# Performance work log

Hardware: AMD Instinct MI355X
Metric: run time of the kernel (lower is better)

## Reference

```python
import jax, jax.numpy as jnp
import numpy as np

PIECES = 64  # self.plane


def _proj(f, w1, b1, w2, b2):
    # Projection: fc2(relu(fc1(f))), final_relu=False
    h = jax.nn.relu(f @ w1 + b1)
    return h @ w2 + b2


def _cf(img, param, pieces):
    # img: [B,3,H,W], param: [B,3,P]
    # total[b,c,h,w] = sum_i clamp(img - i/P, 0, 1/P) * param[b,c,i], then * P / sum_i param
    grid = jnp.arange(pieces, dtype=img.dtype) / pieces            # [P]
    clipped = jnp.clip(img[..., None] - grid, 0.0, 1.0 / pieces)   # [B,3,H,W,P]
    total = jnp.einsum('bchwp,bcp->bchw', clipped, param)
    norm = pieces / (jnp.sum(param, axis=-1) + 1e-30)              # [B,3]
    return total * norm[:, :, None, None]


def setup_inputs() -> dict:
    key = jax.random.key(0)
    ks = jax.random.split(key, 11)
    B, H, W = 8, 256, 256
    s = 0.05
    return {
        'x': jax.random.uniform(ks[0], (B, 3, H, W), jnp.float32),
        'f_feature': jax.random.normal(ks[1], (B, 512), jnp.float32),
        'b_feature': jax.random.normal(ks[2], (B, 512), jnp.float32),
        # stacked weights for [fc_f_1, fc_b_1, fc_f_s, fc_b_s]
        'proj_w1': jax.random.normal(ks[3], (4, 512, 192), jnp.float32) * s,
        'proj_b1': jax.random.normal(ks[4], (4, 192), jnp.float32) * s,
        'proj_w2': jax.random.normal(ks[5], (4, 192, 192), jnp.float32) * s,
        'proj_b2': jax.random.normal(ks[6], (4, 192), jnp.float32) * s,
        'fc_w1': jax.random.normal(ks[7], (576, 192), jnp.float32) * s,
        'fc_b1': jax.random.normal(ks[8], (192,), jnp.float32) * s,
        'fc_w2': jax.random.normal(ks[9], (192, 192), jnp.float32) * s,
        'fc_b2': jax.random.normal(ks[10], (192,), jnp.float32) * s,
    }


def reference(x, f_feature, b_feature, proj_w1, proj_b1, proj_w2, proj_b2,
              fc_w1, fc_b1, fc_w2, fc_b2):
    B = x.shape[0]
    # rgb_to_grayscale with 3 output channels (ITU-R 601 weights)
    gw = jnp.array([0.299, 0.587, 0.114], dtype=x.dtype)
    gray = jnp.broadcast_to(jnp.einsum('bchw,c->bhw', x, gw)[:, None], x.shape)

    # four stacked Projections: inputs [f, b, f, b]
    feats = jnp.stack([f_feature, b_feature, f_feature, b_feature])       # [4,B,512]
    h = jax.nn.relu(jnp.einsum('kbi,kio->kbo', feats, proj_w1) + proj_b1[:, None, :])
    outs = jnp.einsum('kbo,koq->kbq', h, proj_w2) + proj_b2[:, None, :]   # [4,B,192]
    param_f, param_b = outs[0], outs[1]
    param_s = outs[2] + outs[3]

    cat = jnp.concatenate([param_f, param_b, param_s], axis=1)            # [B,576]
    param = _proj(cat, fc_w1, fc_b1, fc_w2, fc_b2)                        # [B,192]

    p_all = param.reshape(B, 3, PIECES)
    p_f = param_f.reshape(B, 3, PIECES)
    p_b = param_b.reshape(B, 3, PIECES)

    return (_cf(x, p_all, PIECES), _cf(gray, p_f, PIECES), _cf(gray, p_b, PIECES))
```

## Files before the change

kernel.cpp:

```cpp
#include <hip/hip_runtime.h>

#define HWSZ 65536
#define PLANE (3 * HWSZ)
#define OUTSTRIDE (8 * PLANE)
#define MAGIC 0x13572468

__global__ __launch_bounds__(384) void k_mlp(
    const float* __restrict__ f, const float* __restrict__ bf,
    const float* __restrict__ pw1, const float* __restrict__ pb1,
    const float* __restrict__ pw2, const float* __restrict__ pb2,
    const float* __restrict__ fw1, const float* __restrict__ fb1,
    const float* __restrict__ fw2, const float* __restrict__ fb2,
    float* __restrict__ ws) {
  __shared__ float smem[2304];
  int t = threadIdx.x, blk = blockIdx.x;

  float* outs    = ws;
  float* partial = ws + 8192;
  int* fbase = (int*)(ws + 16384);

  int k = blk >> 3, b = blk & 7;
  {
    int q = t % 48, s = t / 48;
    float* sf  = smem;
    float* red = smem + 512;
    float* sh  = smem + 2048;

    const float* feat = ((k & 1) ? bf : f) + b * 512;
    for (int i = t; i < 512; i += 384) sf[i] = feat[i];
    __syncthreads();

    {
      const float4* w = (const float4*)(pw1 + (size_t)k * (512 * 192));
      float4 acc = {0.f, 0.f, 0.f, 0.f};
      int i0 = s * 64;
      for (int r = 0; r < 4; ++r) {
        float4 wv[16];
#pragma unroll
        for (int j = 0; j < 16; ++j)
          wv[j] = w[(size_t)(i0 + r * 16 + j) * 48 + q];
#pragma unroll
        for (int j = 0; j < 16; ++j) {
          float v = sf[i0 + r * 16 + j];
          acc.x = fmaf(v, wv[j].x, acc.x); acc.y = fmaf(v, wv[j].y, acc.y);
          acc.z = fmaf(v, wv[j].z, acc.z); acc.w = fmaf(v, wv[j].w, acc.w);
        }
      }
      ((float4*)(red + s * 192))[q] = acc;
    }
    __syncthreads();
    if (t < 192) {
      float a = pb1[k * 192 + t];
#pragma unroll
      for (int s2 = 0; s2 < 8; ++s2) a += red[s2 * 192 + t];
      sh[t] = fmaxf(a, 0.f);
    }
    __syncthreads();
    {
      const float4* w = (const float4*)(pw2 + (size_t)k * (192 * 192));
      float4 acc = {0.f, 0.f, 0.f, 0.f};
      int i0 = s * 24;
      for (int r = 0; r < 2; ++r) {
        float4 wv[12];
#pragma unroll
        for (int j = 0; j < 12; ++j)
          wv[j] = w[(size_t)(i0 + r * 12 + j) * 48 + q];
#pragma unroll
        for (int j = 0; j < 12; ++j) {
          float v = sh[i0 + r * 12 + j];
          acc.x = fmaf(v, wv[j].x, acc.x); acc.y = fmaf(v, wv[j].y, acc.y);
          acc.z = fmaf(v, wv[j].z, acc.z); acc.w = fmaf(v, wv[j].w, acc.w);
        }
      }
      ((float4*)(red + s * 192))[q] = acc;
    }
    __syncthreads();
    if (t < 192) {
      float a = pb2[k * 192 + t];
#pragma unroll
      for (int s2 = 0; s2 < 8; ++s2) a += red[s2 * 192 + t];
      outs[(k * 8 + b) * 192 + t] = a;
    }
    __syncthreads();
    if (t == 0) {
      __threadfence();
      atomicExch(&fbase[blk * 16], MAGIC);
    }
  }

  int b2 = blk & 7, c4 = blk >> 3, ob2 = c4 * 48;
  int q = t % 12, s = t / 12;
  int q2 = t % 48, s2 = t / 48;

  float4 wv1[18];
  {
    const float4* w = (const float4*)fw1;
    int i0 = s * 18;
#pragma unroll
    for (int j = 0; j < 18; ++j)
      wv1[j] = w[(size_t)(i0 + j) * 48 + (ob2 >> 2) + q];
  }
  float4 wv2[6];
  {
    const float4* w = (const float4*)fw2;
#pragma unroll
    for (int j = 0; j < 6; ++j)
      wv2[j] = w[(size_t)(ob2 + s2 * 6 + j) * 48 + q2];
  }

  if (t < 4) {
    while (atomicAdd(&fbase[(t * 8 + b2) * 16], 0) != MAGIC)
      __builtin_amdgcn_s_sleep(2);
  }
  __syncthreads();
  if (t == 0) __threadfence();
  __syncthreads();

  {
    float* sc  = smem;
    float* red = smem + 576;
    for (int idx = t; idx < 576; idx += 384) {
      float v;
      if (idx < 192)      v = outs[(0 * 8 + b2) * 192 + idx];
      else if (idx < 384) v = outs[(1 * 8 + b2) * 192 + (idx - 192)];
      else                v = outs[(2 * 8 + b2) * 192 + (idx - 384)] +
                              outs[(3 * 8 + b2) * 192 + (idx - 384)];
      sc[idx] = v;
    }
    __syncthreads();
    {
      float4 acc = {0.f, 0.f, 0.f, 0.f};
      int i0 = s * 18;
#pragma unroll
      for (int j = 0; j < 18; ++j) {
        float v = sc[i0 + j];
        acc.x = fmaf(v, wv1[j].x, acc.x); acc.y = fmaf(v, wv1[j].y, acc.y);
        acc.z = fmaf(v, wv1[j].z, acc.z); acc.w = fmaf(v, wv1[j].w, acc.w);
      }
      ((float4*)(red + s * 48))[q] = acc;
    }
    __syncthreads();
    if (t < 48) {
      float a = fb1[ob2 + t];
#pragma unroll
      for (int s3 = 0; s3 < 32; ++s3) a += red[s3 * 48 + t];
      smem[t] = fmaxf(a, 0.f);
    }
    __syncthreads();
    {
      float4 acc = {0.f, 0.f, 0.f, 0.f};
#pragma unroll
      for (int j = 0; j < 6; ++j) {
        float v = smem[s2 * 6 + j];
        acc.x = fmaf(v, wv2[j].x, acc.x); acc.y = fmaf(v, wv2[j].y, acc.y);
        acc.z = fmaf(v, wv2[j].z, acc.z); acc.w = fmaf(v, wv2[j].w, acc.w);
      }
      ((float4*)(red + s2 * 192))[q2] = acc;
    }
    __syncthreads();
    if (t < 192) {
      float a = (c4 == 0) ? fb2[t] : 0.f;
#pragma unroll
      for (int s3 = 0; s3 < 8; ++s3) a += red[s3 * 192 + t];
      partial[(c4 * 8 + b2) * 192 + t] = a;
    }
  }
}

__global__ __launch_bounds__(256) void k_render(
    const float* __restrict__ x, const float* __restrict__ ws,
    float* __restrict__ out) {
  int b = blockIdx.y, t = threadIdx.x;
  int wave = t >> 6, lane = t & 63;
  const float* outs    = ws;
  const float* partial = ws + 8192;
  __shared__ float2 tab[576];

  int s4a = blockIdx.x * 512 + t, s4b = s4a + 256;
  const float* xb = x + (size_t)b * PLANE;
  float4 vr0 = ((const float4*)(xb))[s4a];
  float4 vr1 = ((const float4*)(xb))[s4b];
  float4 vg0 = ((const float4*)(xb + HWSZ))[s4a];
  float4 vg1 = ((const float4*)(xb + HWSZ))[s4b];
  float4 vb0 = ((const float4*)(xb + 2 * HWSZ))[s4a];
  float4 vb1 = ((const float4*)(xb + 2 * HWSZ))[s4b];

  for (int cur = wave; cur < 9; cur += 4) {
    int oi = cur / 3, c = cur - oi * 3;
    float p;
    if (oi == 0) {
      const float* pp = partial + b * 192 + c * 64;
      p = pp[lane] + pp[1536 + lane] + pp[3072 + lane] + pp[4608 + lane];
    } else {
      p = outs[((oi - 1) * 8 + b) * 192 + c * 64 + lane];
    }
    float v = p;
#pragma unroll
    for (int d = 1; d < 64; d <<= 1) {
      float n = __shfl_up(v, d, 64);
      if (lane >= d) v += n;
    }
    float total = __shfl(v, 63, 64);
    float norm = 64.f / (total + 1e-30f);
    tab[cur * 64 + lane] = make_float2((v - p) * 0.015625f * norm, p * norm);
  }
  __syncthreads();

  auto idx_of = [&](float v, int& kk, float& tt) {
    int k = (int)(v * 64.f);
    k = k < 0 ? 0 : (k > 63 ? 63 : k);
    kk = k;
    tt = v - (float)k * 0.015625f;
  };
  auto evk = [&](int cur, int k, float tt) -> float {
    float2 e = tab[cur * 64 + k];
    return fmaf(tt, e.y, e.x);
  };
  auto ev4 = [&](int cur, float4 v) -> float4 {
    int k; float tt; float4 r;
    idx_of(v.x, k, tt); r.x = evk(cur, k, tt);
    idx_of(v.y, k, tt); r.y = evk(cur, k, tt);
    idx_of(v.z, k, tt); r.z = evk(cur, k, tt);
    idx_of(v.w, k, tt); r.w = evk(cur, k, tt);
    return r;
  };

  float* o0 = out + (size_t)b * PLANE;
  float* o1 = out + OUTSTRIDE + (size_t)b * PLANE;
  float* o2 = out + 2 * OUTSTRIDE + (size_t)b * PLANE;

  auto process = [&](int s4, float4 vr, float4 vg, float4 vb) {
    float4 gr;
    gr.x = fmaf(0.299f, vr.x, fmaf(0.587f, vg.x, 0.114f * vb.x));
    gr.y = fmaf(0.299f, vr.y, fmaf(0.587f, vg.y, 0.114f * vb.y));
    gr.z = fmaf(0.299f, vr.z, fmaf(0.587f, vg.z, 0.114f * vb.z));
    gr.w = fmaf(0.299f, vr.w, fmaf(0.587f, vg.w, 0.114f * vb.w));

    ((float4*)(o0))[s4]            = ev4(0, vr);
    ((float4*)(o0 + HWSZ))[s4]     = ev4(1, vg);
    ((float4*)(o0 + 2 * HWSZ))[s4] = ev4(2, vb);

    int kx, ky, kz, kw; float tx, ty, tz, tw;
    idx_of(gr.x, kx, tx); idx_of(gr.y, ky, ty);
    idx_of(gr.z, kz, tz); idx_of(gr.w, kw, tw);
#pragma unroll
    for (int c = 0; c < 3; ++c) {
      float4 r;
      r.x = evk(3 + c, kx, tx); r.y = evk(3 + c, ky, ty);
      r.z = evk(3 + c, kz, tz); r.w = evk(3 + c, kw, tw);
      ((float4*)(o1 + c * HWSZ))[s4] = r;
    }
#pragma unroll
    for (int c = 0; c < 3; ++c) {
      float4 r;
      r.x = evk(6 + c, kx, tx); r.y = evk(6 + c, ky, ty);
      r.z = evk(6 + c, kz, tz); r.w = evk(6 + c, kw, tw);
      ((float4*)(o2 + c * HWSZ))[s4] = r;
    }
  };

  process(s4a, vr0, vg0, vb0);
  process(s4b, vr1, vg1, vb1);
}

extern "C" void kernel_launch(void* const* d_in, const int* in_sizes, int n_in,
                              void* d_out, int out_size, void* d_ws, size_t ws_size,
                              hipStream_t stream) {
  const float* x   = (const float*)d_in[0];
  const float* f   = (const float*)d_in[1];
  const float* bf  = (const float*)d_in[2];
  const float* pw1 = (const float*)d_in[3];
  const float* pb1 = (const float*)d_in[4];
  const float* pw2 = (const float*)d_in[5];
  const float* pb2 = (const float*)d_in[6];
  const float* fw1 = (const float*)d_in[7];
  const float* fb1 = (const float*)d_in[8];
  const float* fw2 = (const float*)d_in[9];
  const float* fb2 = (const float*)d_in[10];
  float* out = (float*)d_out;
  float* ws  = (float*)d_ws;

  k_mlp<<<32, 384, 0, stream>>>(f, bf, pw1, pb1, pw2, pb2, fw1, fb1, fw2,
                                fb2, ws);
  dim3 grid(32, 8);
  k_render<<<grid, 256, 0, stream>>>(x, ws, out);
}
```

Measured before the change: 97.92 us.

## Split projection MLP hidden dim across two blocks to double MLP parallelism

The projection MLP kernel now launches 64 blocks instead of 32, each computing half of the fc1 hidden units for one (projection, batch) pair and writing a partial fc2 result. The two halves and the fc2 bias are summed by the consumers (the final-fc stage and the render kernel). Only half the blocks continue into the final-fc stage, and each now spin-waits on 8 flags instead of 4. This aims to cut per-block weight streaming latency on the critical path, at the cost of extra partial reads and more inter-block flag synchronization.

```diff
diff --git a/kernel.cpp b/kernel.cpp
--- a/kernel.cpp
+++ b/kernel.cpp
@@ -15,13 +15,13 @@
   __shared__ float smem[2304];
   int t = threadIdx.x, blk = blockIdx.x;
 
-  float* outs    = ws;
-  float* partial = ws + 8192;
-  int* fbase = (int*)(ws + 16384);
-
-  int k = blk >> 3, b = blk & 7;
+  float* pA      = ws;
+  float* partial = ws + 12288;
+  int* fbase = (int*)(ws + 20480);
+
+  int s = blk & 7, b = blk >> 3;
+  int k = s >> 1, half = s & 1, o0 = half * 96;
   {
-    int q = t % 48, s = t / 48;
     float* sf  = smem;
     float* red = smem + 512;
     float* sh  = smem + 2048;
@@ -31,14 +31,16 @@
     __syncthreads();
 
     {
+      int q = t % 24, sr = t / 24;
       const float4* w = (const float4*)(pw1 + (size_t)k * (512 * 192));
+      int icol = half * 24 + q;
       float4 acc = {0.f, 0.f, 0.f, 0.f};
-      int i0 = s * 64;
-      for (int r = 0; r < 4; ++r) {
+      int i0 = sr * 32;
+      for (int r = 0; r < 2; ++r) {
         float4 wv[16];
 #pragma unroll
         for (int j = 0; j < 16; ++j)
-          wv[j] = w[(size_t)(i0 + r * 16 + j) * 48 + q];
+          wv[j] = w[(size_t)(i0 + r * 16 + j) * 48 + icol];
 #pragma unroll
         for (int j = 0; j < 16; ++j) {
           float v = sf[i0 + r * 16 + j];
@@ -46,40 +48,38 @@
           acc.z = fmaf(v, wv[j].z, acc.z); acc.w = fmaf(v, wv[j].w, acc.w);
         }
       }
-      ((float4*)(red + s * 192))[q] = acc;
-    }
-    __syncthreads();
-    if (t < 192) {
-      float a = pb1[k * 192 + t];
-#pragma unroll
-      for (int s2 = 0; s2 < 8; ++s2) a += red[s2 * 192 + t];
+      ((float4*)(red + sr * 96))[q] = acc;
+    }
+    __syncthreads();
+    if (t < 96) {
+      float a = pb1[k * 192 + o0 + t];
+#pragma unroll
+      for (int s2 = 0; s2 < 16; ++s2) a += red[s2 * 96 + t];
       sh[t] = fmaxf(a, 0.f);
     }
     __syncthreads();
     {
+      int q2 = t % 48, s2 = t / 48;
       const float4* w = (const float4*)(pw2 + (size_t)k * (192 * 192));
       float4 acc = {0.f, 0.f, 0.f, 0.f};
-      int i0 = s * 24;
-      for (int r = 0; r < 2; ++r) {
-        float4 wv[12];
-#pragma unroll
-        for (int j = 0; j < 12; ++j)
-          wv[j] = w[(size_t)(i0 + r * 12 + j) * 48 + q];
-#pragma unroll
-        for (int j = 0; j < 12; ++j) {
-          float v = sh[i0 + r * 12 + j];
-          acc.x = fmaf(v, wv[j].x, acc.x); acc.y = fmaf(v, wv[j].y, acc.y);
-          acc.z = fmaf(v, wv[j].z, acc.z); acc.w = fmaf(v, wv[j].w, acc.w);
-        }
-      }
-      ((float4*)(red + s * 192))[q] = acc;
+      float4 wv[12];
+#pragma unroll
+      for (int j = 0; j < 12; ++j)
+        wv[j] = w[(size_t)(o0 + s2 * 12 + j) * 48 + q2];
+#pragma unroll
+      for (int j = 0; j < 12; ++j) {
+        float v = sh[s2 * 12 + j];
+        acc.x = fmaf(v, wv[j].x, acc.x); acc.y = fmaf(v, wv[j].y, acc.y);
+        acc.z = fmaf(v, wv[j].z, acc.z); acc.w = fmaf(v, wv[j].w, acc.w);
+      }
+      ((float4*)(red + s2 * 192))[q2] = acc;
     }
     __syncthreads();
     if (t < 192) {
-      float a = pb2[k * 192 + t];
-#pragma unroll
-      for (int s2 = 0; s2 < 8; ++s2) a += red[s2 * 192 + t];
-      outs[(k * 8 + b) * 192 + t] = a;
+      float a = 0.f;
+#pragma unroll
+      for (int s3 = 0; s3 < 8; ++s3) a += red[s3 * 192 + t];
+      pA[((k * 8 + b) * 2 + half) * 192 + t] = a;
     }
     __syncthreads();
     if (t == 0) {
@@ -88,17 +88,19 @@
     }
   }
 
-  int b2 = blk & 7, c4 = blk >> 3, ob2 = c4 * 48;
-  int q = t % 12, s = t / 12;
+  if (s >= 4) return;
+
+  int b2 = b, c4 = s, ob2 = c4 * 48;
+  int q = t % 12, sb = t / 12;
   int q2 = t % 48, s2 = t / 48;
 
   float4 wv1[18];
   {
     const float4* w = (const float4*)fw1;
-    int i0 = s * 18;
+    int i0 = sb * 18;
 #pragma unroll
     for (int j = 0; j < 18; ++j)
-      wv1[j] = w[(size_t)(i0 + j) * 48 + (ob2 >> 2) + q];
+      wv1[j] = w[(size_t)(i0 + j) * 48 + c4 * 12 + q];
   }
   float4 wv2[6];
   {
@@ -108,8 +110,8 @@
       wv2[j] = w[(size_t)(ob2 + s2 * 6 + j) * 48 + q2];
   }
 
-  if (t < 4) {
-    while (atomicAdd(&fbase[(t * 8 + b2) * 16], 0) != MAGIC)
+  if (t < 8) {
+    while (atomicAdd(&fbase[((b2 << 3) + t) * 16], 0) != MAGIC)
       __builtin_amdgcn_s_sleep(2);
   }
   __syncthreads();
@@ -121,23 +123,33 @@
     float* red = smem + 576;
     for (int idx = t; idx < 576; idx += 384) {
       float v;
-      if (idx < 192)      v = outs[(0 * 8 + b2) * 192 + idx];
-      else if (idx < 384) v = outs[(1 * 8 + b2) * 192 + (idx - 192)];
-      else                v = outs[(2 * 8 + b2) * 192 + (idx - 384)] +
-                              outs[(3 * 8 + b2) * 192 + (idx - 384)];
+      if (idx < 192) {
+        const float* p0 = pA + ((0 * 8 + b2) * 2) * 192;
+        v = p0[idx] + p0[192 + idx] + pb2[idx];
+      } else if (idx < 384) {
+        int jj = idx - 192;
+        const float* p1 = pA + ((1 * 8 + b2) * 2) * 192;
+        v = p1[jj] + p1[192 + jj] + pb2[192 + jj];
+      } else {
+        int jj = idx - 384;
+        const float* p2 = pA + ((2 * 8 + b2) * 2) * 192;
+        const float* p3 = pA + ((3 * 8 + b2) * 2) * 192;
+        v = p2[jj] + p2[192 + jj] + p3[jj] + p3[192 + jj] +
+            pb2[384 + jj] + pb2[576 + jj];
+      }
       sc[idx] = v;
     }
     __syncthreads();
     {
       float4 acc = {0.f, 0.f, 0.f, 0.f};
-      int i0 = s * 18;
+      int i0 = sb * 18;
 #pragma unroll
       for (int j = 0; j < 18; ++j) {
         float v = sc[i0 + j];
         acc.x = fmaf(v, wv1[j].x, acc.x); acc.y = fmaf(v, wv1[j].y, acc.y);
         acc.z = fmaf(v, wv1[j].z, acc.z); acc.w = fmaf(v, wv1[j].w, acc.w);
       }
-      ((float4*)(red + s * 48))[q] = acc;
+      ((float4*)(red + sb * 48))[q] = acc;
     }
     __syncthreads();
     if (t < 48) {
@@ -169,11 +181,11 @@
 
 __global__ __launch_bounds__(256) void k_render(
     const float* __restrict__ x, const float* __restrict__ ws,
-    float* __restrict__ out) {
+    const float* __restrict__ pb2, float* __restrict__ out) {
   int b = blockIdx.y, t = threadIdx.x;
   int wave = t >> 6, lane = t & 63;
-  const float* outs    = ws;
-  const float* partial = ws + 8192;
+  const float* pA      = ws;
+  const float* partial = ws + 12288;
   __shared__ float2 tab[576];
 
   int s4a = blockIdx.x * 512 + t, s4b = s4a + 256;
@@ -192,7 +204,8 @@
       const float* pp = partial + b * 192 + c * 64;
       p = pp[lane] + pp[1536 + lane] + pp[3072 + lane] + pp[4608 + lane];
     } else {
-      p = outs[((oi - 1) * 8 + b) * 192 + c * 64 + lane];
+      const float* pa = pA + (((oi - 1) * 8 + b) * 2) * 192 + c * 64;
+      p = pa[lane] + pa[192 + lane] + pb2[(oi - 1) * 192 + c * 64 + lane];
     }
     float v = p;
 #pragma unroll
@@ -280,8 +293,8 @@
   float* out = (float*)d_out;
   float* ws  = (float*)d_ws;
 
-  k_mlp<<<32, 384, 0, stream>>>(f, bf, pw1, pb1, pw2, pb2, fw1, fb1, fw2,
+  k_mlp<<<64, 384, 0, stream>>>(f, bf, pw1, pb1, pw2, pb2, fw1, fb1, fw2,
                                 fb2, ws);
   dim3 grid(32, 8);
-  k_render<<<grid, 256, 0, stream>>>(x, ws, out);
+  k_render<<<grid, 256, 0, stream>>>(x, ws, pb2, out);
 }
```

Measured after the change: 94.44 us, median of 2. 1.04x faster.
